# Kernel optimization log

Measured on AMD Instinct MI355X. Metric: run time of the kernel, lower is better.

## Reference

```python
import jax, jax.numpy as jnp
import numpy as np

B, N, T, J = 64, 64, 32, 128   # batch, num_hnodes, time_win, feature dim
IN_F, OUT_F = 4096, 256


def setup_inputs() -> dict:
    key = jax.random.key(0)
    k1, k2, k3 = jax.random.split(key, 3)
    inp = jax.random.normal(k1, (B, T, J, N), dtype=jnp.float32)
    indices = jax.random.randint(k2, (B, N, T), 0, IN_F, dtype=jnp.int64)
    full_weight = jax.random.normal(k3, (OUT_F, IN_F), dtype=jnp.float32)
    return {"input": inp, "indices": indices, "full_weight": full_weight}


def reference(input, indices, full_weight):
    # Gather columns of full_weight per (b, n, t): [OUT_F, B, N, T]
    w = full_weight[:, indices]
    # einsum 'bijk,lbki->bijl' with i=time, j=feat, k=hnodes, l=out
    y = jnp.einsum('btjn,lbnt->btjl', input, w)
    return y
```

## Files before the change

kernel.cpp:

```cpp
#include <hip/hip_runtime.h>
#include <stdint.h>

#define Bv   64
#define Tv   32
#define Jv   128
#define Nv   64
#define Lv   256
#define INFv 4096

typedef __attribute__((ext_vector_type(8))) short  short8;
typedef __attribute__((ext_vector_type(4))) float  floatx4;

__device__ __forceinline__ unsigned int f2bf(float f) {
  union { float f; unsigned int u; } v; v.f = f;
  unsigned int r = v.u + 0x7fffu + ((v.u >> 16) & 1u);
  return r >> 16;
}

__global__ __launch_bounds__(256) void wt_transpose_kernel(
    const float* __restrict__ w, unsigned short* __restrict__ wt) {
  int i_base = blockIdx.x * 16;
  int wave = threadIdx.x >> 6;
  int lane = threadIdx.x & 63;
  #pragma unroll
  for (int r = 0; r < 4; ++r) {
    int i = i_base + wave * 4 + r;
    unsigned int b0 = f2bf(w[(size_t)(4 * lane + 0) * INFv + i]);
    unsigned int b1 = f2bf(w[(size_t)(4 * lane + 1) * INFv + i]);
    unsigned int b2 = f2bf(w[(size_t)(4 * lane + 2) * INFv + i]);
    unsigned int b3 = f2bf(w[(size_t)(4 * lane + 3) * INFv + i]);
    uint2 u;
    u.x = b0 | (b1 << 16);
    u.y = b2 | (b3 << 16);
    *(uint2*)(wt + (size_t)i * Lv + 4 * lane) = u;
  }
}

template <int USE_WT>
__global__ __launch_bounds__(256, 3) void masklin_kernel(
    const float* __restrict__ x, const int* __restrict__ idx,
    const unsigned short* __restrict__ wt, const float* __restrict__ wfull,
    float* __restrict__ y) {
  const int blk  = blockIdx.x;
  const int bt   = blk >> 1;
  const int jh   = blk & 1;
  const int b    = bt >> 5;
  const int t    = bt & 31;
  const int tid  = threadIdx.x;
  const int wave = tid >> 6;
  const int lane = tid & 63;
  const int m    = lane & 15;
  const int qd   = lane >> 4;
  const int lbase = wave << 6;
  const int jbase = jh << 6;

  const int* idxp = idx + ((b << 6) * Tv) + t;
  int rows[16];
  #pragma unroll
  for (int ks = 0; ks < 2; ++ks)
    #pragma unroll
    for (int j = 0; j < 8; ++j)
      rows[ks * 8 + j] = idxp[((ks << 5) + (qd << 3) + j) * Tv];

  short8 afr[2][4];
  #pragma unroll
  for (int ks = 0; ks < 2; ++ks) {
    #pragma unroll
    for (int lt = 0; lt < 4; ++lt) {
      const int lcol = lbase + (lt << 4) + m;
      unsigned int e[8];
      #pragma unroll
      for (int j = 0; j < 8; ++j) {
        if (USE_WT) {
          e[j] = wt[(unsigned int)rows[ks * 8 + j] * Lv + lcol];
        } else {
          e[j] = f2bf(wfull[(size_t)lcol * INFv + rows[ks * 8 + j]]);
        }
      }
      uint4 v;
      v.x = e[0] | (e[1] << 16);
      v.y = e[2] | (e[3] << 16);
      v.z = e[4] | (e[5] << 16);
      v.w = e[6] | (e[7] << 16);
      afr[ks][lt] = *(short8*)&v;
    }
  }

  const float* xt = x + (size_t)bt * (Jv * Nv) + (size_t)jbase * Nv;
  short8 bfr[2][4];
  #pragma unroll
  for (int jt = 0; jt < 4; ++jt) {
    const float* xp = xt + (size_t)((jt << 4) + m) * Nv + (qd << 3);
    #pragma unroll
    for (int ks = 0; ks < 2; ++ks) {
      float4 a0 = *(const float4*)(xp + (ks << 5));
      float4 a1 = *(const float4*)(xp + (ks << 5) + 4);
      uint4 v;
      v.x = f2bf(a0.x) | (f2bf(a0.y) << 16);
      v.y = f2bf(a0.z) | (f2bf(a0.w) << 16);
      v.z = f2bf(a1.x) | (f2bf(a1.y) << 16);
      v.w = f2bf(a1.z) | (f2bf(a1.w) << 16);
      bfr[ks][jt] = *(short8*)&v;
    }
  }

  floatx4 acc[4][4];
  #pragma unroll
  for (int lt = 0; lt < 4; ++lt)
    #pragma unroll
    for (int jt = 0; jt < 4; ++jt)
      acc[lt][jt] = (floatx4){0.f, 0.f, 0.f, 0.f};

  #pragma unroll
  for (int ks = 0; ks < 2; ++ks)
    #pragma unroll
    for (int jt = 0; jt < 4; ++jt)
      #pragma unroll
      for (int lt = 0; lt < 4; ++lt)
        acc[lt][jt] = __builtin_amdgcn_mfma_f32_16x16x32_bf16(
            afr[ks][lt], bfr[ks][jt], acc[lt][jt], 0, 0, 0);

  float* yt = y + (size_t)bt * (Jv * Lv);
  #pragma unroll
  for (int jt = 0; jt < 4; ++jt) {
    float* yr = yt + (size_t)(jbase + (jt << 4) + m) * Lv + lbase + (qd << 2);
    #pragma unroll
    for (int lt = 0; lt < 4; ++lt)
      __builtin_nontemporal_store(acc[lt][jt], (floatx4*)(yr + (lt << 4)));
  }
}

extern "C" void kernel_launch(void* const* d_in, const int* in_sizes, int n_in,
                              void* d_out, int out_size, void* d_ws, size_t ws_size,
                              hipStream_t stream) {
  const float* x    = (const float*)d_in[0];
  const int*   idx  = (const int*)d_in[1];
  const float* w    = (const float*)d_in[2];
  float*       y    = (float*)d_out;

  const size_t wt_bytes = (size_t)INFv * Lv * sizeof(unsigned short);
  int use_wt = (d_ws != nullptr && ws_size >= wt_bytes) ? 1 : 0;
  unsigned short* wt = (unsigned short*)d_ws;

  if (use_wt) {
    wt_transpose_kernel<<<256, 256, 0, stream>>>(w, wt);
    masklin_kernel<1><<<Bv * Tv * 2, 256, 0, stream>>>(x, idx, wt, w, y);
  } else {
    masklin_kernel<0><<<Bv * Tv * 2, 256, 0, stream>>>(x, idx, (const unsigned short*)nullptr, w, y);
  }
}
```

Measured before the change: 360.2 us.

## Stage converted input tile in swizzled LDS and share gathered indices across waves

Before, each of the four waves loaded and converted the same 64x64 input slice to bf16 on its own, and each lane read 16 indices from global memory. Now the block loads the slice once with coalesced float4 reads, converts it, and writes it to XOR-swizzled shared memory. It also loads the 64 indices into shared memory once per block. The weight gather and B-fragment reads now happen per k-step inside the MFMA loop. This cuts redundant global traffic and conversion work, at the cost of a __syncthreads, extra LDS use that may lower occupancy, and less overlap between gather latency and the MFMAs.

```diff
diff --git a/kernel.cpp b/kernel.cpp
--- a/kernel.cpp
+++ b/kernel.cpp
@@ -41,6 +41,9 @@
     const float* __restrict__ x, const int* __restrict__ idx,
     const unsigned short* __restrict__ wt, const float* __restrict__ wfull,
     float* __restrict__ y) {
+  __shared__ __align__(16) unsigned short lA[64 * Nv];
+  __shared__ int idxs[Nv];
+
   const int blk  = blockIdx.x;
   const int bt   = blk >> 1;
   const int jh   = blk & 1;
@@ -54,55 +57,23 @@
   const int lbase = wave << 6;
   const int jbase = jh << 6;
 
-  const int* idxp = idx + ((b << 6) * Tv) + t;
-  int rows[16];
-  #pragma unroll
-  for (int ks = 0; ks < 2; ++ks)
-    #pragma unroll
-    for (int j = 0; j < 8; ++j)
-      rows[ks * 8 + j] = idxp[((ks << 5) + (qd << 3) + j) * Tv];
-
-  short8 afr[2][4];
-  #pragma unroll
-  for (int ks = 0; ks < 2; ++ks) {
-    #pragma unroll
-    for (int lt = 0; lt < 4; ++lt) {
-      const int lcol = lbase + (lt << 4) + m;
-      unsigned int e[8];
-      #pragma unroll
-      for (int j = 0; j < 8; ++j) {
-        if (USE_WT) {
-          e[j] = wt[(unsigned int)rows[ks * 8 + j] * Lv + lcol];
-        } else {
-          e[j] = f2bf(wfull[(size_t)lcol * INFv + rows[ks * 8 + j]]);
-        }
-      }
-      uint4 v;
-      v.x = e[0] | (e[1] << 16);
-      v.y = e[2] | (e[3] << 16);
-      v.z = e[4] | (e[5] << 16);
-      v.w = e[6] | (e[7] << 16);
-      afr[ks][lt] = *(short8*)&v;
-    }
-  }
+  if (tid < Nv) idxs[tid] = idx[(b * Nv + tid) * Tv + t];
 
   const float* xt = x + (size_t)bt * (Jv * Nv) + (size_t)jbase * Nv;
-  short8 bfr[2][4];
   #pragma unroll
-  for (int jt = 0; jt < 4; ++jt) {
-    const float* xp = xt + (size_t)((jt << 4) + m) * Nv + (qd << 3);
-    #pragma unroll
-    for (int ks = 0; ks < 2; ++ks) {
-      float4 a0 = *(const float4*)(xp + (ks << 5));
-      float4 a1 = *(const float4*)(xp + (ks << 5) + 4);
-      uint4 v;
-      v.x = f2bf(a0.x) | (f2bf(a0.y) << 16);
-      v.y = f2bf(a0.z) | (f2bf(a0.w) << 16);
-      v.z = f2bf(a1.x) | (f2bf(a1.y) << 16);
-      v.w = f2bf(a1.z) | (f2bf(a1.w) << 16);
-      bfr[ks][jt] = *(short8*)&v;
-    }
+  for (int it = 0; it < 2; ++it) {
+    int O = tid + it * 256;
+    int j = O >> 3, c = O & 7;
+    const float4* p = (const float4*)(xt + (size_t)O * 8);
+    float4 a0 = p[0], a1 = p[1];
+    uint4 v;
+    v.x = f2bf(a0.x) | (f2bf(a0.y) << 16);
+    v.y = f2bf(a0.z) | (f2bf(a0.w) << 16);
+    v.z = f2bf(a1.x) | (f2bf(a1.y) << 16);
+    v.w = f2bf(a1.z) | (f2bf(a1.w) << 16);
+    *(uint4*)&lA[j * 64 + ((c ^ (j & 7)) << 3)] = v;
   }
+  __syncthreads();
 
   floatx4 acc[4][4];
   #pragma unroll
@@ -112,13 +83,48 @@
       acc[lt][jt] = (floatx4){0.f, 0.f, 0.f, 0.f};
 
   #pragma unroll
-  for (int ks = 0; ks < 2; ++ks)
+  for (int ks = 0; ks < 2; ++ks) {
+    int rows[8];
+    #pragma unroll
+    for (int j = 0; j < 8; ++j)
+      rows[j] = idxs[(ks << 5) + (qd << 3) + j];
+
+    short8 afr[4];
+    #pragma unroll
+    for (int lt = 0; lt < 4; ++lt) {
+      const int lcol = lbase + (lt << 4) + m;
+      unsigned int e[8];
+      #pragma unroll
+      for (int j = 0; j < 8; ++j) {
+        if (USE_WT) {
+          e[j] = wt[(unsigned int)rows[j] * Lv + lcol];
+        } else {
+          e[j] = f2bf(wfull[(size_t)lcol * INFv + rows[j]]);
+        }
+      }
+      uint4 v;
+      v.x = e[0] | (e[1] << 16);
+      v.y = e[2] | (e[3] << 16);
+      v.z = e[4] | (e[5] << 16);
+      v.w = e[6] | (e[7] << 16);
+      afr[lt] = *(short8*)&v;
+    }
+
+    const int chunk = (ks << 2) + qd;
+    short8 bfr[4];
+    #pragma unroll
+    for (int jt = 0; jt < 4; ++jt) {
+      int j = (jt << 4) + m;
+      bfr[jt] = *(const short8*)&lA[j * 64 + ((chunk ^ (j & 7)) << 3)];
+    }
+
     #pragma unroll
     for (int jt = 0; jt < 4; ++jt)
       #pragma unroll
       for (int lt = 0; lt < 4; ++lt)
         acc[lt][jt] = __builtin_amdgcn_mfma_f32_16x16x32_bf16(
-            afr[ks][lt], bfr[ks][jt], acc[lt][jt], 0, 0, 0);
+            afr[lt], bfr[jt], acc[lt][jt], 0, 0, 0);
+  }
 
   float* yt = y + (size_t)bt * (Jv * Lv);
   #pragma unroll
```

After: 339.6 us. 1.06x faster.
